# Performance work log

Measured on AMD Instinct MI355X. Metric: run time of the kernel, lower is better.

The kernel has to match this reference:

```python
import jax, jax.numpy as jnp
import numpy as np

EPS = 1e-12
LORA_RANK = 16

def setup_inputs() -> dict:
    key = jax.random.key(0)
    ks = jax.random.split(key, 7)
    bs, sq, din, dout = 8, 2048, 2048, 2048
    n_tasks, n_splits, n_skills, r = 32, 1, 8, LORA_RANK
    return {
        'x': jax.random.normal(ks[0], (bs, sq, din), dtype=jnp.float32),
        'W': jax.random.normal(ks[1], (dout, din), dtype=jnp.float32) * (1.0 / np.sqrt(din)),
        'b': jax.random.normal(ks[2], (dout,), dtype=jnp.float32) * 0.02,
        'module_logits': jax.random.normal(ks[3], (n_tasks, n_splits * n_skills), dtype=jnp.float32) * 0.001,
        'A': jax.random.normal(ks[4], (n_splits, n_skills, din // n_splits, r), dtype=jnp.float32) * 0.02,
        'B': jax.random.normal(ks[5], (n_splits, n_skills, r, dout // n_splits), dtype=jnp.float32) * 0.02,
        'tasks': jax.random.randint(ks[6], (bs,), 0, n_tasks),
    }

def reference(x, W, b, module_logits, A, B, tasks):
    bs, sq, din = x.shape
    n_splits, n_skills, _, r = A.shape
    dout = W.shape[0]
    # Polytropon selector (eval mode): sigmoid + normalize over skills
    probs = jax.nn.sigmoid(module_logits[tasks]).reshape(bs, n_splits, n_skills)
    probs = probs / (probs.sum(-1, keepdims=True) + EPS)  # [bs, p, t]
    # WeightedSum combinor: per-example skill mixture of LoRA params
    A_c = jnp.einsum('bpt,ptir->bpir', probs, A)  # [bs, p, din/p, r]
    B_c = jnp.einsum('bpt,ptro->bpro', probs, B)  # [bs, p, r, dout/p]
    # LoRA forward: reshape to per-example [din, r] and [r, dout]
    A_r = A_c.reshape(bs, din, r)
    B_r = jnp.transpose(B_c, (0, 2, 1, 3)).reshape(bs, r, dout)
    lora = jnp.einsum('bsr,bro->bso', jnp.einsum('bsi,bir->bsr', x, A_r), B_r)
    base = jnp.einsum('bsi,oi->bso', x, W) + b
    return base + lora * (1.0 / r)
```

## Files before the change

kernel.cpp:

```cpp
#include <hip/hip_runtime.h>

typedef __attribute__((ext_vector_type(4))) float f32x4;
typedef __attribute__((ext_vector_type(8))) short bf16x8;

__device__ __forceinline__ unsigned short f2b(float f) {
  unsigned u = __float_as_uint(f);
  u = (u + 0x7FFFu + ((u >> 16) & 1u)) >> 16;
  return (unsigned short)u;
}

#define BAR() asm volatile("s_barrier" ::: "memory")
#define VMCNT(N) asm volatile("s_waitcnt vmcnt(" #N ")" ::: "memory")

__global__ void combine_kernel(const float* __restrict__ logits,
                               const int*   __restrict__ tasks,
                               const float* __restrict__ A,
                               const float* __restrict__ B,
                               unsigned short* __restrict__ Art,
                               unsigned short* __restrict__ Brt)
{
  int idx = blockIdx.x * 256 + threadIdx.x;
  int b = idx >> 11;
  int i = idx & 2047;
  if (b >= 8) return;
  int task = tasks[b];
  float p[8]; float s = 0.f;
  #pragma unroll
  for (int t = 0; t < 8; ++t) {
    float l = logits[task * 8 + t];
    float e = 1.f / (1.f + __expf(-l));
    p[t] = e; s += e;
  }
  float inv = 1.f / (s + 1e-12f);
  #pragma unroll
  for (int t = 0; t < 8; ++t) p[t] *= inv;

  float ar[16];
  #pragma unroll
  for (int r = 0; r < 16; ++r) ar[r] = 0.f;
  for (int t = 0; t < 8; ++t) {
    const float* ap = A + ((size_t)t * 2048 + i) * 16;
    float pt = p[t];
    #pragma unroll
    for (int r = 0; r < 16; ++r) ar[r] += pt * ap[r];
  }
  #pragma unroll
  for (int r = 0; r < 16; ++r)
    Art[((size_t)b * 16 + r) * 2048 + i] = f2b(ar[r]);

  float br[16];
  #pragma unroll
  for (int r = 0; r < 16; ++r) br[r] = 0.f;
  for (int t = 0; t < 8; ++t) {
    float pt = p[t];
    #pragma unroll
    for (int r = 0; r < 16; ++r) br[r] += pt * B[((size_t)t * 16 + r) * 2048 + i];
  }
  #pragma unroll
  for (int r = 0; r < 16; ++r)
    Brt[((size_t)b * 2048 + i) * 16 + r] = f2b(br[r] * 0.0625f);
}

__global__ void prep_kernel(const float* __restrict__ x,
                            const unsigned short* __restrict__ Art,
                            const float* __restrict__ W,
                            unsigned short* __restrict__ Wb,
                            unsigned short* __restrict__ xb,
                            unsigned short* __restrict__ xa)
{
  __shared__ float red[4][16][16];
  int blk = blockIdx.x;
  int tid = threadIdx.x;
  if (blk >= 1024) {
    int idx0 = (blk - 1024) * 256 + tid;
    #pragma unroll
    for (int c = 0; c < 32; ++c) {
      size_t i = ((size_t)idx0 + (size_t)c * 32768) * 4;
      f32x4 v = *(const f32x4*)(W + i);
      ushort4 o;
      o.x = f2b(v.x); o.y = f2b(v.y); o.z = f2b(v.z); o.w = f2b(v.w);
      *(ushort4*)(Wb + i) = o;
    }
    return;
  }
  int lane = tid & 63, wv = tid >> 6;
  int lr = lane & 15, hi = lane >> 4;
  int rowbase = blk * 16;
  int batch = rowbase >> 11;
  int row = rowbase + lr;
  f32x4 acc; acc.x = 0.f; acc.y = 0.f; acc.z = 0.f; acc.w = 0.f;
  const float* xrow = x + (size_t)row * 2048 + wv * 512 + hi * 8;
  unsigned short* xbrow = xb + (size_t)row * 2048 + wv * 512 + hi * 8;
  const unsigned short* artrow = Art + ((size_t)batch * 16 + lr) * 2048 + wv * 512 + hi * 8;
  #pragma unroll
  for (int ks = 0; ks < 16; ++ks) {
    f32x4 v0 = *(const f32x4*)(xrow + ks * 32);
    f32x4 v1 = *(const f32x4*)(xrow + ks * 32 + 4);
    bf16x8 av;
    av[0] = (short)f2b(v0.x); av[1] = (short)f2b(v0.y);
    av[2] = (short)f2b(v0.z); av[3] = (short)f2b(v0.w);
    av[4] = (short)f2b(v1.x); av[5] = (short)f2b(v1.y);
    av[6] = (short)f2b(v1.z); av[7] = (short)f2b(v1.w);
    *(bf16x8*)(xbrow + ks * 32) = av;
    bf16x8 bv = *(const bf16x8*)(artrow + ks * 32);
    acc = __builtin_amdgcn_mfma_f32_16x16x32_bf16(av, bv, acc, 0, 0, 0);
  }
  #pragma unroll
  for (int j = 0; j < 4; ++j) red[wv][hi * 4 + j][lr] = acc[j];
  __syncthreads();
  int rr = tid >> 4, cc = tid & 15;
  float s = red[0][rr][cc] + red[1][rr][cc] + red[2][rr][cc] + red[3][rr][cc];
  xa[(size_t)(rowbase + rr) * 16 + cc] = f2b(s);
}

__global__ __launch_bounds__(512, 2)
void gemm_kernel(const unsigned short* __restrict__ xb,
                 const unsigned short* __restrict__ Wb,
                 const float* __restrict__ bias,
                 const unsigned short* __restrict__ xa,
                 const unsigned short* __restrict__ Brt,
                 float* __restrict__ out)
{
  __shared__ __align__(16) char lds[131072];
  const int tid = threadIdx.x;
  const int lane = tid & 63;
  const int wv = tid >> 6;
  const int wr = wv >> 2, wc = wv & 3;
  const int lr = lane & 15, hi = lane >> 4;
  const int hi16 = hi * 16;

  const int bid = blockIdx.x;
  const int swz = (bid & 7) * 64 + (bid >> 3);
  const int tm = swz >> 3, tn = swz & 7;
  const int rowbase = tm * 256, colbase = tn * 256;

  const int row0 = tid >> 3;
  const int cb0 = (tid & 7) * 16;
  const int scb_e = (cb0 ^ ((row0 & 7) << 4)) >> 1;
  const int rb5 = ((row0 >> 5) << 6) + (row0 & 31);

#define GL16(LDSOFF, GPTR) \
  __builtin_amdgcn_global_load_lds((const __attribute__((address_space(1))) unsigned int*)(GPTR), \
      (__attribute__((address_space(3))) unsigned int*)(lds + (LDSOFF)), 16, 0, 0)

#define STAGE_A(MH, DBUF, KOFF) { \
  const unsigned short* g_ = xb + (size_t)(rowbase + (MH)*64 + row0) * 2048 + (KOFF) + scb_e; \
  GL16((DBUF)*65536 + (MH)*16384 + tid*16, g_); \
  GL16((DBUF)*65536 + (MH)*16384 + 8192 + tid*16, g_ + 128*2048); \
}
#define STAGE_B(NH, DBUF, KOFF) { \
  const unsigned short* g_ = Wb + (size_t)(colbase + (NH)*32 + rb5) * 2048 + (KOFF) + scb_e; \
  GL16((DBUF)*65536 + 32768 + (NH)*16384 + tid*16, g_); \
  GL16((DBUF)*65536 + 32768 + (NH)*16384 + 8192 + tid*16, g_ + 128*2048); \
}

#define READ_A(MH) \
  _Pragma("unroll") \
  for (int mf = 0; mf < 4; ++mf) { \
    int ar_ = (MH)*128 + wr*64 + mf*16 + lr; \
    _Pragma("unroll") \
    for (int kk = 0; kk < 2; ++kk) \
      a[mf][kk] = *(const bf16x8*)(Ab + ar_*128 + ((kk*64 + hi16) ^ ((ar_&7)<<4))); \
  }
#define READ_B(NH, BREG) \
  _Pragma("unroll") \
  for (int nf = 0; nf < 2; ++nf) { \
    int br_ = (NH)*128 + wc*32 + nf*16 + lr; \
    _Pragma("unroll") \
    for (int kk = 0; kk < 2; ++kk) \
      BREG[nf][kk] = *(const bf16x8*)(Bb + br_*128 + ((kk*64 + hi16) ^ ((br_&7)<<4))); \
  }
#define MFMA_BLOCK(MH, NH, BREG) \
  __builtin_amdgcn_s_setprio(1); \
  _Pragma("unroll") \
  for (int mf = 0; mf < 4; ++mf) \
    _Pragma("unroll") \
    for (int nf = 0; nf < 2; ++nf) \
      _Pragma("unroll") \
      for (int kk = 0; kk < 2; ++kk) \
        acc[(MH)*4+mf][(NH)*2+nf] = __builtin_amdgcn_mfma_f32_16x16x32_bf16( \
            a[mf][kk], BREG[nf][kk], acc[(MH)*4+mf][(NH)*2+nf], 0, 0, 0); \
  __builtin_amdgcn_s_setprio(0);

  f32x4 acc[8][4];
  #pragma unroll
  for (int i = 0; i < 8; ++i)
    #pragma unroll
    for (int n = 0; n < 4; ++n) { acc[i][n].x = 0.f; acc[i][n].y = 0.f; acc[i][n].z = 0.f; acc[i][n].w = 0.f; }

  bf16x8 a[4][2], b0[2][2], b1[2][2];

  STAGE_A(0, 0, 0);
  STAGE_B(0, 0, 0);
  STAGE_A(1, 0, 0);
  STAGE_B(1, 0, 0);
  STAGE_A(0, 1, 64);
  STAGE_B(0, 1, 64);
  VMCNT(8);
  BAR();

  for (int kt = 0; kt < 32; ++kt) {
    const int buf = kt & 1, nbuf = buf ^ 1;
    const char* Ab = lds + buf * 65536;
    const char* Bb = Ab + 32768;
    const int k1 = (kt + 1) * 64, k2 = (kt + 2) * 64;

    READ_A(0);
    READ_B(0, b0);
    if (kt < 31) STAGE_A(1, nbuf, k1);
    BAR();
    MFMA_BLOCK(0, 0, b0);
    if (kt < 31) { VMCNT(6); } else { VMCNT(0); }
    BAR();

    READ_B(1, b1);
    if (kt < 31) STAGE_B(1, nbuf, k1);
    BAR();
    MFMA_BLOCK(0, 1, b1);
    BAR();

    READ_A(1);
    if (kt < 30) STAGE_A(0, buf, k2);
    BAR();
    MFMA_BLOCK(1, 0, b0);
    BAR();

    if (kt < 30) STAGE_B(0, buf, k2);
    BAR();
    MFMA_BLOCK(1, 1, b1);
    if (kt < 30) { VMCNT(6); }
    else if (kt == 30) { VMCNT(4); }
    BAR();
  }

  const int batch = rowbase >> 11;
  bf16x8 zf = (bf16x8)(short)0;
  bf16x8 av[8], bv[4];
  #pragma unroll
  for (int i = 0; i < 8; ++i) {
    if (hi < 2)
      av[i] = *(const bf16x8*)(xa + (size_t)(rowbase + wr * 128 + i * 16 + lr) * 16 + hi * 8);
    else
      av[i] = zf;
  }
  #pragma unroll
  for (int n = 0; n < 4; ++n) {
    if (hi < 2)
      bv[n] = *(const bf16x8*)(Brt + ((size_t)batch * 2048 + colbase + wc * 64 + n * 16 + lr) * 16 + hi * 8);
    else
      bv[n] = zf;
  }
  #pragma unroll
  for (int i = 0; i < 8; ++i)
    #pragma unroll
    for (int n = 0; n < 4; ++n)
      acc[i][n] = __builtin_amdgcn_mfma_f32_16x16x32_bf16(av[i], bv[n], acc[i][n], 0, 0, 0);

  #pragma unroll
  for (int n = 0; n < 4; ++n) {
    int col = colbase + wc * 64 + n * 16 + lr;
    float bbv = bias[col];
    #pragma unroll
    for (int i = 0; i < 8; ++i) {
      int r0 = rowbase + wr * 128 + i * 16 + hi * 4;
      #pragma unroll
      for (int j = 0; j < 4; ++j)
        out[(size_t)(r0 + j) * 2048 + col] = acc[i][n][j] + bbv;
    }
  }
#undef GL16
#undef STAGE_A
#undef STAGE_B
#undef READ_A
#undef READ_B
#undef MFMA_BLOCK
}

extern "C" void kernel_launch(void* const* d_in, const int* in_sizes, int n_in,
                              void* d_out, int out_size, void* d_ws, size_t ws_size,
                              hipStream_t stream) {
  const float* x      = (const float*)d_in[0];
  const float* W      = (const float*)d_in[1];
  const float* bias   = (const float*)d_in[2];
  const float* logits = (const float*)d_in[3];
  const float* A      = (const float*)d_in[4];
  const float* B      = (const float*)d_in[5];
  const int*   tasks  = (const int*)d_in[6];
  float* out = (float*)d_out;

  char* ws = (char*)d_ws;
  unsigned short* xb  = (unsigned short*)(ws);
  unsigned short* Wb  = (unsigned short*)(ws + 67108864);
  unsigned short* xa  = (unsigned short*)(ws + 67108864 + 8388608);
  unsigned short* Art = (unsigned short*)(ws + 67108864 + 8388608 + 524288);
  unsigned short* Brt = (unsigned short*)(ws + 67108864 + 8388608 + 1048576);

  combine_kernel<<<64, 256, 0, stream>>>(logits, tasks, A, B, Art, Brt);
  prep_kernel<<<1152, 256, 0, stream>>>(x, Art, W, Wb, xb, xa);
  gemm_kernel<<<512, 512, 0, stream>>>(xb, Wb, bias, xa, Brt, out);
}
```

Measured before the change: 193.3 us.

## Switch GEMM to 32x32x16 MFMA with whole-tile staging and simpler pipeline

Result: slower. 201.2 us (+4.1%).

```diff
diff --git a/kernel.cpp b/kernel.cpp
--- a/kernel.cpp
+++ b/kernel.cpp
@@ -1,6 +1,7 @@
 #include <hip/hip_runtime.h>
 
 typedef __attribute__((ext_vector_type(4))) float f32x4;
+typedef __attribute__((ext_vector_type(16))) float f32x16;
 typedef __attribute__((ext_vector_type(8))) short bf16x8;
 
 __device__ __forceinline__ unsigned short f2b(float f) {
@@ -126,154 +127,125 @@
   const int lane = tid & 63;
   const int wv = tid >> 6;
   const int wr = wv >> 2, wc = wv & 3;
-  const int lr = lane & 15, hi = lane >> 4;
-  const int hi16 = hi * 16;
+  const int rl = lane & 31, lh = lane >> 5;
 
   const int bid = blockIdx.x;
   const int swz = (bid & 7) * 64 + (bid >> 3);
   const int tm = swz >> 3, tn = swz & 7;
   const int rowbase = tm * 256, colbase = tn * 256;
 
-  const int row0 = tid >> 3;
-  const int cb0 = (tid & 7) * 16;
-  const int scb_e = (cb0 ^ ((row0 & 7) << 4)) >> 1;
-  const int rb5 = ((row0 >> 5) << 6) + (row0 & 31);
+  const int srow = tid >> 3;
+  const int scb_e = ((((tid & 7) * 16) ^ ((srow & 7) << 4)) >> 1);
+
+  int koff[4];
+  #pragma unroll
+  for (int ks = 0; ks < 4; ++ks) koff[ks] = (((ks * 2 + lh) ^ (rl & 7)) << 4);
+  int aro[4], bro[2];
+  #pragma unroll
+  for (int mf = 0; mf < 4; ++mf) aro[mf] = (wr * 128 + mf * 32 + rl) * 128;
+  #pragma unroll
+  for (int nf = 0; nf < 2; ++nf) bro[nf] = (wc * 64 + nf * 32 + rl) * 128;
 
 #define GL16(LDSOFF, GPTR) \
   __builtin_amdgcn_global_load_lds((const __attribute__((address_space(1))) unsigned int*)(GPTR), \
       (__attribute__((address_space(3))) unsigned int*)(lds + (LDSOFF)), 16, 0, 0)
 
-#define STAGE_A(MH, DBUF, KOFF) { \
-  const unsigned short* g_ = xb + (size_t)(rowbase + (MH)*64 + row0) * 2048 + (KOFF) + scb_e; \
-  GL16((DBUF)*65536 + (MH)*16384 + tid*16, g_); \
-  GL16((DBUF)*65536 + (MH)*16384 + 8192 + tid*16, g_ + 128*2048); \
-}
-#define STAGE_B(NH, DBUF, KOFF) { \
-  const unsigned short* g_ = Wb + (size_t)(colbase + (NH)*32 + rb5) * 2048 + (KOFF) + scb_e; \
-  GL16((DBUF)*65536 + 32768 + (NH)*16384 + tid*16, g_); \
-  GL16((DBUF)*65536 + 32768 + (NH)*16384 + 8192 + tid*16, g_ + 128*2048); \
-}
-
-#define READ_A(MH) \
+#define STAGE_TILE(DBUF, KOFFS) { \
+  const unsigned short* ga_ = xb + (size_t)(rowbase + srow) * 2048 + (KOFFS) + scb_e; \
+  const unsigned short* gb_ = Wb + (size_t)(colbase + srow) * 2048 + (KOFFS) + scb_e; \
+  GL16((DBUF) * 65536 + tid * 16, ga_); \
+  GL16((DBUF) * 65536 + 8192 + tid * 16, ga_ + 64 * 2048); \
+  GL16((DBUF) * 65536 + 16384 + tid * 16, ga_ + 128 * 2048); \
+  GL16((DBUF) * 65536 + 24576 + tid * 16, ga_ + 192 * 2048); \
+  GL16((DBUF) * 65536 + 32768 + tid * 16, gb_); \
+  GL16((DBUF) * 65536 + 40960 + tid * 16, gb_ + 64 * 2048); \
+  GL16((DBUF) * 65536 + 49152 + tid * 16, gb_ + 128 * 2048); \
+  GL16((DBUF) * 65536 + 57344 + tid * 16, gb_ + 192 * 2048); \
+}
+
+#define RD(S, AV, BV) { \
   _Pragma("unroll") \
-  for (int mf = 0; mf < 4; ++mf) { \
-    int ar_ = (MH)*128 + wr*64 + mf*16 + lr; \
-    _Pragma("unroll") \
-    for (int kk = 0; kk < 2; ++kk) \
-      a[mf][kk] = *(const bf16x8*)(Ab + ar_*128 + ((kk*64 + hi16) ^ ((ar_&7)<<4))); \
-  }
-#define READ_B(NH, BREG) \
+  for (int mf = 0; mf < 4; ++mf) AV[mf] = *(const bf16x8*)(Ab + aro[mf] + koff[S]); \
   _Pragma("unroll") \
-  for (int nf = 0; nf < 2; ++nf) { \
-    int br_ = (NH)*128 + wc*32 + nf*16 + lr; \
-    _Pragma("unroll") \
-    for (int kk = 0; kk < 2; ++kk) \
-      BREG[nf][kk] = *(const bf16x8*)(Bb + br_*128 + ((kk*64 + hi16) ^ ((br_&7)<<4))); \
-  }
-#define MFMA_BLOCK(MH, NH, BREG) \
+  for (int nf = 0; nf < 2; ++nf) BV[nf] = *(const bf16x8*)(Bb + bro[nf] + koff[S]); \
+}
+
+#define MM(AV, BV) \
   __builtin_amdgcn_s_setprio(1); \
   _Pragma("unroll") \
   for (int mf = 0; mf < 4; ++mf) \
     _Pragma("unroll") \
     for (int nf = 0; nf < 2; ++nf) \
-      _Pragma("unroll") \
-      for (int kk = 0; kk < 2; ++kk) \
-        acc[(MH)*4+mf][(NH)*2+nf] = __builtin_amdgcn_mfma_f32_16x16x32_bf16( \
-            a[mf][kk], BREG[nf][kk], acc[(MH)*4+mf][(NH)*2+nf], 0, 0, 0); \
+      acc[mf][nf] = __builtin_amdgcn_mfma_f32_32x32x16_bf16(AV[mf], BV[nf], acc[mf][nf], 0, 0, 0); \
   __builtin_amdgcn_s_setprio(0);
 
-  f32x4 acc[8][4];
-  #pragma unroll
-  for (int i = 0; i < 8; ++i)
-    #pragma unroll
-    for (int n = 0; n < 4; ++n) { acc[i][n].x = 0.f; acc[i][n].y = 0.f; acc[i][n].z = 0.f; acc[i][n].w = 0.f; }
-
-  bf16x8 a[4][2], b0[2][2], b1[2][2];
-
-  STAGE_A(0, 0, 0);
-  STAGE_B(0, 0, 0);
-  STAGE_A(1, 0, 0);
-  STAGE_B(1, 0, 0);
-  STAGE_A(0, 1, 64);
-  STAGE_B(0, 1, 64);
+  f32x16 acc[4][2];
+  #pragma unroll
+  for (int i = 0; i < 4; ++i)
+    #pragma unroll
+    for (int n = 0; n < 2; ++n)
+      #pragma unroll
+      for (int r = 0; r < 16; ++r) acc[i][n][r] = 0.f;
+
+  bf16x8 av0[4], bv0[2], av1[4], bv1[2];
+
+  STAGE_TILE(0, 0);
+  STAGE_TILE(1, 64);
   VMCNT(8);
   BAR();
 
   for (int kt = 0; kt < 32; ++kt) {
-    const int buf = kt & 1, nbuf = buf ^ 1;
+    const int buf = kt & 1;
     const char* Ab = lds + buf * 65536;
     const char* Bb = Ab + 32768;
-    const int k1 = (kt + 1) * 64, k2 = (kt + 2) * 64;
-
-    READ_A(0);
-    READ_B(0, b0);
-    if (kt < 31) STAGE_A(1, nbuf, k1);
+
+    RD(0, av0, bv0);
+    RD(1, av1, bv1);
+    MM(av0, bv0);
+    RD(2, av0, bv0);
+    MM(av1, bv1);
+    RD(3, av1, bv1);
     BAR();
-    MFMA_BLOCK(0, 0, b0);
-    if (kt < 31) { VMCNT(6); } else { VMCNT(0); }
+    MM(av0, bv0);
+    if (kt < 30) STAGE_TILE(buf, (kt + 2) * 64);
+    MM(av1, bv1);
+    if (kt < 30) { VMCNT(8); }
+    else if (kt == 30) { VMCNT(0); }
     BAR();
-
-    READ_B(1, b1);
-    if (kt < 31) STAGE_B(1, nbuf, k1);
-    BAR();
-    MFMA_BLOCK(0, 1, b1);
-    BAR();
-
-    READ_A(1);
-    if (kt < 30) STAGE_A(0, buf, k2);
-    BAR();
-    MFMA_BLOCK(1, 0, b0);
-    BAR();
-
-    if (kt < 30) STAGE_B(0, buf, k2);
-    BAR();
-    MFMA_BLOCK(1, 1, b1);
-    if (kt < 30) { VMCNT(6); }
-    else if (kt == 30) { VMCNT(4); }
-    BAR();
   }
 
   const int batch = rowbase >> 11;
-  bf16x8 zf = (bf16x8)(short)0;
-  bf16x8 av[8], bv[4];
-  #pragma unroll
-  for (int i = 0; i < 8; ++i) {
-    if (hi < 2)
-      av[i] = *(const bf16x8*)(xa + (size_t)(rowbase + wr * 128 + i * 16 + lr) * 16 + hi * 8);
-    else
-      av[i] = zf;
-  }
-  #pragma unroll
-  for (int n = 0; n < 4; ++n) {
-    if (hi < 2)
-      bv[n] = *(const bf16x8*)(Brt + ((size_t)batch * 2048 + colbase + wc * 64 + n * 16 + lr) * 16 + hi * 8);
-    else
-      bv[n] = zf;
-  }
-  #pragma unroll
-  for (int i = 0; i < 8; ++i)
-    #pragma unroll
-    for (int n = 0; n < 4; ++n)
-      acc[i][n] = __builtin_amdgcn_mfma_f32_16x16x32_bf16(av[i], bv[n], acc[i][n], 0, 0, 0);
-
-  #pragma unroll
-  for (int n = 0; n < 4; ++n) {
-    int col = colbase + wc * 64 + n * 16 + lr;
+  bf16x8 la[4], lb[2];
+  #pragma unroll
+  for (int i = 0; i < 4; ++i)
+    la[i] = *(const bf16x8*)(xa + (size_t)(rowbase + wr * 128 + i * 32 + rl) * 16 + lh * 8);
+  #pragma unroll
+  for (int n = 0; n < 2; ++n)
+    lb[n] = *(const bf16x8*)(Brt + ((size_t)batch * 2048 + colbase + wc * 64 + n * 32 + rl) * 16 + lh * 8);
+  #pragma unroll
+  for (int i = 0; i < 4; ++i)
+    #pragma unroll
+    for (int n = 0; n < 2; ++n)
+      acc[i][n] = __builtin_amdgcn_mfma_f32_32x32x16_bf16(la[i], lb[n], acc[i][n], 0, 0, 0);
+
+  #pragma unroll
+  for (int n = 0; n < 2; ++n) {
+    int col = colbase + wc * 64 + n * 32 + rl;
     float bbv = bias[col];
     #pragma unroll
-    for (int i = 0; i < 8; ++i) {
-      int r0 = rowbase + wr * 128 + i * 16 + hi * 4;
+    for (int i = 0; i < 4; ++i) {
+      int r0 = rowbase + wr * 128 + i * 32 + 4 * lh;
       #pragma unroll
-      for (int j = 0; j < 4; ++j)
-        out[(size_t)(r0 + j) * 2048 + col] = acc[i][n][j] + bbv;
+      for (int r = 0; r < 16; ++r) {
+        int row = r0 + (r & 3) + 8 * (r >> 2);
+        out[(size_t)row * 2048 + col] = acc[i][n][r] + bbv;
+      }
     }
   }
 #undef GL16
-#undef STAGE_A
-#undef STAGE_B
-#undef READ_A
-#undef READ_B
-#undef MFMA_BLOCK
+#undef STAGE_TILE
+#undef RD
+#undef MM
 }
 
 extern "C" void kernel_launch(void* const* d_in, const int* in_sizes, int n_in,
```

## Load W fragments directly to registers and halve LDS to A-only double buffer

Applied to the files above, without the earlier changes.

Result: slower. 546.1 us (+182.6%).

```diff
diff --git a/kernel.cpp b/kernel.cpp
--- a/kernel.cpp
+++ b/kernel.cpp
@@ -121,7 +121,7 @@
                  const unsigned short* __restrict__ Brt,
                  float* __restrict__ out)
 {
-  __shared__ __align__(16) char lds[131072];
+  __shared__ __align__(16) char lds[65536];
   const int tid = threadIdx.x;
   const int lane = tid & 63;
   const int wv = tid >> 6;
@@ -130,131 +130,104 @@
   const int hi16 = hi * 16;
 
   const int bid = blockIdx.x;
-  const int swz = (bid & 7) * 64 + (bid >> 3);
-  const int tm = swz >> 3, tn = swz & 7;
+  const int tn = bid & 7, tm = bid >> 3;
   const int rowbase = tm * 256, colbase = tn * 256;
 
-  const int row0 = tid >> 3;
-  const int cb0 = (tid & 7) * 16;
-  const int scb_e = (cb0 ^ ((row0 & 7) << 4)) >> 1;
-  const int rb5 = ((row0 >> 5) << 6) + (row0 & 31);
+  const int srow = tid >> 3;
+  const int scb_e = ((((tid & 7) * 16) ^ ((srow & 7) << 4)) >> 1);
+
+  const unsigned short* bgbase = Wb + (size_t)(colbase + wc * 64 + lr) * 2048 + hi * 8;
 
 #define GL16(LDSOFF, GPTR) \
   __builtin_amdgcn_global_load_lds((const __attribute__((address_space(1))) unsigned int*)(GPTR), \
       (__attribute__((address_space(3))) unsigned int*)(lds + (LDSOFF)), 16, 0, 0)
 
-#define STAGE_A(MH, DBUF, KOFF) { \
-  const unsigned short* g_ = xb + (size_t)(rowbase + (MH)*64 + row0) * 2048 + (KOFF) + scb_e; \
-  GL16((DBUF)*65536 + (MH)*16384 + tid*16, g_); \
-  GL16((DBUF)*65536 + (MH)*16384 + 8192 + tid*16, g_ + 128*2048); \
-}
-#define STAGE_B(NH, DBUF, KOFF) { \
-  const unsigned short* g_ = Wb + (size_t)(colbase + (NH)*32 + rb5) * 2048 + (KOFF) + scb_e; \
-  GL16((DBUF)*65536 + 32768 + (NH)*16384 + tid*16, g_); \
-  GL16((DBUF)*65536 + 32768 + (NH)*16384 + 8192 + tid*16, g_ + 128*2048); \
-}
-
-#define READ_A(MH) \
+#define STAGE_A(DBUF, KOFFS) { \
+  const unsigned short* ga_ = xb + (size_t)(rowbase + srow) * 2048 + (KOFFS) + scb_e; \
+  GL16((DBUF) * 32768 + tid * 16, ga_); \
+  GL16((DBUF) * 32768 + 8192 + tid * 16, ga_ + 64 * 2048); \
+  GL16((DBUF) * 32768 + 16384 + tid * 16, ga_ + 128 * 2048); \
+  GL16((DBUF) * 32768 + 24576 + tid * 16, ga_ + 192 * 2048); \
+}
+
+#define LOADB(BREG, KOFFS) \
   _Pragma("unroll") \
-  for (int mf = 0; mf < 4; ++mf) { \
-    int ar_ = (MH)*128 + wr*64 + mf*16 + lr; \
+  for (int nf = 0; nf < 4; ++nf) \
     _Pragma("unroll") \
     for (int kk = 0; kk < 2; ++kk) \
-      a[mf][kk] = *(const bf16x8*)(Ab + ar_*128 + ((kk*64 + hi16) ^ ((ar_&7)<<4))); \
-  }
-#define READ_B(NH, BREG) \
+      BREG[nf * 2 + kk] = *(const bf16x8*)(bgbase + (size_t)nf * 16 * 2048 + (KOFFS) + kk * 32);
+
+#define RD_A(KK, AV) \
   _Pragma("unroll") \
-  for (int nf = 0; nf < 2; ++nf) { \
-    int br_ = (NH)*128 + wc*32 + nf*16 + lr; \
-    _Pragma("unroll") \
-    for (int kk = 0; kk < 2; ++kk) \
-      BREG[nf][kk] = *(const bf16x8*)(Bb + br_*128 + ((kk*64 + hi16) ^ ((br_&7)<<4))); \
-  }
-#define MFMA_BLOCK(MH, NH, BREG) \
+  for (int mf = 0; mf < 8; ++mf) { \
+    int ar_ = wr * 128 + mf * 16 + lr; \
+    AV[mf] = *(const bf16x8*)(Ab + ar_ * 128 + (((KK) * 64 + hi16) ^ ((ar_ & 7) << 4))); \
+  }
+
+#define MM(AV, BREG, KK) \
   __builtin_amdgcn_s_setprio(1); \
   _Pragma("unroll") \
-  for (int mf = 0; mf < 4; ++mf) \
+  for (int mf = 0; mf < 8; ++mf) \
     _Pragma("unroll") \
-    for (int nf = 0; nf < 2; ++nf) \
-      _Pragma("unroll") \
-      for (int kk = 0; kk < 2; ++kk) \
-        acc[(MH)*4+mf][(NH)*2+nf] = __builtin_amdgcn_mfma_f32_16x16x32_bf16( \
-            a[mf][kk], BREG[nf][kk], acc[(MH)*4+mf][(NH)*2+nf], 0, 0, 0); \
+    for (int nf = 0; nf < 4; ++nf) \
+      acc[mf][nf] = __builtin_amdgcn_mfma_f32_16x16x32_bf16( \
+          AV[mf], BREG[nf * 2 + (KK)], acc[mf][nf], 0, 0, 0); \
   __builtin_amdgcn_s_setprio(0);
 
+#define KTILE(KT, BCUR, BNXT) { \
+  const char* Ab = lds + ((KT) & 1) * 32768; \
+  RD_A(0, avA); \
+  RD_A(1, avB); \
+  if ((KT) < 31) LOADB(BNXT, ((KT) + 1) * 64); \
+  MM(avA, BCUR, 0); \
+  BAR(); \
+  MM(avB, BCUR, 1); \
+  if ((KT) < 30) STAGE_A((KT) & 1, ((KT) + 2) * 64); \
+  if ((KT) < 30) { VMCNT(4); } else { VMCNT(0); } \
+  BAR(); \
+}
+
   f32x4 acc[8][4];
   #pragma unroll
   for (int i = 0; i < 8; ++i)
     #pragma unroll
     for (int n = 0; n < 4; ++n) { acc[i][n].x = 0.f; acc[i][n].y = 0.f; acc[i][n].z = 0.f; acc[i][n].w = 0.f; }
 
-  bf16x8 a[4][2], b0[2][2], b1[2][2];
-
-  STAGE_A(0, 0, 0);
-  STAGE_B(0, 0, 0);
-  STAGE_A(1, 0, 0);
-  STAGE_B(1, 0, 0);
-  STAGE_A(0, 1, 64);
-  STAGE_B(0, 1, 64);
-  VMCNT(8);
+  bf16x8 avA[8], avB[8], bA[8], bB[8];
+
+  STAGE_A(0, 0);
+  LOADB(bA, 0);
+  STAGE_A(1, 64);
+  VMCNT(4);
   BAR();
 
-  for (int kt = 0; kt < 32; ++kt) {
-    const int buf = kt & 1, nbuf = buf ^ 1;
-    const char* Ab = lds + buf * 65536;
-    const char* Bb = Ab + 32768;
-    const int k1 = (kt + 1) * 64, k2 = (kt + 2) * 64;
-
-    READ_A(0);
-    READ_B(0, b0);
-    if (kt < 31) STAGE_A(1, nbuf, k1);
-    BAR();
-    MFMA_BLOCK(0, 0, b0);
-    if (kt < 31) { VMCNT(6); } else { VMCNT(0); }
-    BAR();
-
-    READ_B(1, b1);
-    if (kt < 31) STAGE_B(1, nbuf, k1);
-    BAR();
-    MFMA_BLOCK(0, 1, b1);
-    BAR();
-
-    READ_A(1);
-    if (kt < 30) STAGE_A(0, buf, k2);
-    BAR();
-    MFMA_BLOCK(1, 0, b0);
-    BAR();
-
-    if (kt < 30) STAGE_B(0, buf, k2);
-    BAR();
-    MFMA_BLOCK(1, 1, b1);
-    if (kt < 30) { VMCNT(6); }
-    else if (kt == 30) { VMCNT(4); }
-    BAR();
+  for (int kt2 = 0; kt2 < 32; kt2 += 2) {
+    KTILE(kt2, bA, bB);
+    KTILE(kt2 + 1, bB, bA);
   }
 
   const int batch = rowbase >> 11;
   bf16x8 zf = (bf16x8)(short)0;
-  bf16x8 av[8], bv[4];
+  bf16x8 ea[8], eb[4];
   #pragma unroll
   for (int i = 0; i < 8; ++i) {
     if (hi < 2)
-      av[i] = *(const bf16x8*)(xa + (size_t)(rowbase + wr * 128 + i * 16 + lr) * 16 + hi * 8);
+      ea[i] = *(const bf16x8*)(xa + (size_t)(rowbase + wr * 128 + i * 16 + lr) * 16 + hi * 8);
     else
-      av[i] = zf;
+      ea[i] = zf;
   }
   #pragma unroll
   for (int n = 0; n < 4; ++n) {
     if (hi < 2)
-      bv[n] = *(const bf16x8*)(Brt + ((size_t)batch * 2048 + colbase + wc * 64 + n * 16 + lr) * 16 + hi * 8);
+      eb[n] = *(const bf16x8*)(Brt + ((size_t)batch * 2048 + colbase + wc * 64 + n * 16 + lr) * 16 + hi * 8);
     else
-      bv[n] = zf;
+      eb[n] = zf;
   }
   #pragma unroll
   for (int i = 0; i < 8; ++i)
     #pragma unroll
     for (int n = 0; n < 4; ++n)
-      acc[i][n] = __builtin_amdgcn_mfma_f32_16x16x32_bf16(av[i], bv[n], acc[i][n], 0, 0, 0);
+      acc[i][n] = __builtin_amdgcn_mfma_f32_16x16x32_bf16(ea[i], eb[n], acc[i][n], 0, 0, 0);
 
   #pragma unroll
   for (int n = 0; n < 4; ++n) {
@@ -270,10 +243,10 @@
   }
 #undef GL16
 #undef STAGE_A
-#undef STAGE_B
-#undef READ_A
-#undef READ_B
-#undef MFMA_BLOCK
+#undef LOADB
+#undef RD_A
+#undef MM
+#undef KTILE
 }
 
 extern "C" void kernel_launch(void* const* d_in, const int* in_sizes, int n_in,
```

## Software-pipeline LDS fragment reads ahead of MFMA blocks in the GEMM main loop

Applied to the files above, without the earlier changes.

Measured after the change: 191.9 us. About the same (-0.7%).

```diff
diff --git a/kernel.cpp b/kernel.cpp
--- a/kernel.cpp
+++ b/kernel.cpp
@@ -113,7 +113,7 @@
   xa[(size_t)(rowbase + rr) * 16 + cc] = f2b(s);
 }
 
-__global__ __launch_bounds__(512, 2)
+__global__ __launch_bounds__(512)
 void gemm_kernel(const unsigned short* __restrict__ xb,
                  const unsigned short* __restrict__ Wb,
                  const float* __restrict__ bias,
@@ -154,21 +154,21 @@
   GL16((DBUF)*65536 + 32768 + (NH)*16384 + 8192 + tid*16, g_ + 128*2048); \
 }
 
-#define READ_A(MH) \
+#define READ_A(MH, ABASE) \
   _Pragma("unroll") \
   for (int mf = 0; mf < 4; ++mf) { \
     int ar_ = (MH)*128 + wr*64 + mf*16 + lr; \
     _Pragma("unroll") \
     for (int kk = 0; kk < 2; ++kk) \
-      a[mf][kk] = *(const bf16x8*)(Ab + ar_*128 + ((kk*64 + hi16) ^ ((ar_&7)<<4))); \
-  }
-#define READ_B(NH, BREG) \
+      a[mf][kk] = *(const bf16x8*)((ABASE) + ar_*128 + ((kk*64 + hi16) ^ ((ar_&7)<<4))); \
+  }
+#define READ_B(NH, BBASE, BREG) \
   _Pragma("unroll") \
   for (int nf = 0; nf < 2; ++nf) { \
     int br_ = (NH)*128 + wc*32 + nf*16 + lr; \
     _Pragma("unroll") \
     for (int kk = 0; kk < 2; ++kk) \
-      BREG[nf][kk] = *(const bf16x8*)(Bb + br_*128 + ((kk*64 + hi16) ^ ((br_&7)<<4))); \
+      BREG[nf][kk] = *(const bf16x8*)((BBASE) + br_*128 + ((kk*64 + hi16) ^ ((br_&7)<<4))); \
   }
 #define MFMA_BLOCK(MH, NH, BREG) \
   __builtin_amdgcn_s_setprio(1); \
@@ -196,65 +196,65 @@
   STAGE_B(1, 0, 0);
   STAGE_A(0, 1, 64);
   STAGE_B(0, 1, 64);
-  VMCNT(8);
+  VMCNT(4);
   BAR();
+  READ_A(0, lds);
+  READ_B(0, lds + 32768, b0);
 
   for (int kt = 0; kt < 32; ++kt) {
     const int buf = kt & 1, nbuf = buf ^ 1;
-    const char* Ab = lds + buf * 65536;
-    const char* Bb = Ab + 32768;
+    const char* Ab  = lds + buf * 65536;
+    const char* Bb  = Ab + 32768;
+    const char* Abn = lds + nbuf * 65536;
+    const char* Bbn = Abn + 32768;
     const int k1 = (kt + 1) * 64, k2 = (kt + 2) * 64;
 
-    READ_A(0);
-    READ_B(0, b0);
+    BAR();
+    READ_B(1, Bb, b1);
     if (kt < 31) STAGE_A(1, nbuf, k1);
+    MFMA_BLOCK(0, 0, b0);
+
     BAR();
-    MFMA_BLOCK(0, 0, b0);
-    if (kt < 31) { VMCNT(6); } else { VMCNT(0); }
+    if (kt < 31) STAGE_B(1, nbuf, k1);
+    MFMA_BLOCK(0, 1, b1);
+    READ_A(1, Ab);
+    if (kt < 31) { VMCNT(4); }
+
     BAR();
-
-    READ_B(1, b1);
-    if (kt < 31) STAGE_B(1, nbuf, k1);
+    if (kt < 30) STAGE_A(0, buf, k2);
+    MFMA_BLOCK(1, 0, b0);
+    if (kt < 31) READ_B(0, Bbn, b0);
+
     BAR();
-    MFMA_BLOCK(0, 1, b1);
-    BAR();
-
-    READ_A(1);
-    if (kt < 30) STAGE_A(0, buf, k2);
-    BAR();
-    MFMA_BLOCK(1, 0, b0);
-    BAR();
-
     if (kt < 30) STAGE_B(0, buf, k2);
-    BAR();
     MFMA_BLOCK(1, 1, b1);
-    if (kt < 30) { VMCNT(6); }
-    else if (kt == 30) { VMCNT(4); }
-    BAR();
+    if (kt < 31) READ_A(0, Abn);
+    if (kt < 30) { VMCNT(4); }
+    else if (kt == 30) { VMCNT(0); }
   }
 
   const int batch = rowbase >> 11;
   bf16x8 zf = (bf16x8)(short)0;
-  bf16x8 av[8], bv[4];
+  bf16x8 ea[8], eb[4];
   #pragma unroll
   for (int i = 0; i < 8; ++i) {
     if (hi < 2)
-      av[i] = *(const bf16x8*)(xa + (size_t)(rowbase + wr * 128 + i * 16 + lr) * 16 + hi * 8);
+      ea[i] = *(const bf16x8*)(xa + (size_t)(rowbase + wr * 128 + i * 16 + lr) * 16 + hi * 8);
     else
-      av[i] = zf;
+      ea[i] = zf;
   }
   #pragma unroll
   for (int n = 0; n < 4; ++n) {
     if (hi < 2)
-      bv[n] = *(const bf16x8*)(Brt + ((size_t)batch * 2048 + colbase + wc * 64 + n * 16 + lr) * 16 + hi * 8);
+      eb[n] = *(const bf16x8*)(Brt + ((size_t)batch * 2048 + colbase + wc * 64 + n * 16 + lr) * 16 + hi * 8);
     else
-      bv[n] = zf;
+      eb[n] = zf;
   }
   #pragma unroll
   for (int i = 0; i < 8; ++i)
     #pragma unroll
     for (int n = 0; n < 4; ++n)
-      acc[i][n] = __builtin_amdgcn_mfma_f32_16x16x32_bf16(av[i], bv[n], acc[i][n], 0, 0, 0);
+      acc[i][n] = __builtin_amdgcn_mfma_f32_16x16x32_bf16(ea[i], eb[n], acc[i][n], 0, 0, 0);
 
   #pragma unroll
   for (int n = 0; n < 4; ++n) {
```
